# Performance work log

Measured on AMD Instinct MI355X. Metric: run time of the kernel, lower is better.

Reference implementation:

```python
import jax, jax.numpy as jnp
import numpy as np

D_MODEL, N_LAYER, VOCAB = 1024, 4, 50280
D_INNER, D_STATE, D_CONV, DT_RANK = 2048, 16, 4, 64
B, L = 1, 1024
EPS = 1e-5


def _rmsnorm(x, w):
    var = jnp.mean(jnp.square(x), axis=-1, keepdims=True)
    return x * jax.lax.rsqrt(var + EPS) * w


def _selective_scan(u, dt, A, Bm, Cm, Dv):
    # u, dt: [b,l,d]; A: [d,n]; Bm, Cm: [b,l,n]; Dv: [d]
    dA = jnp.exp(dt[..., None] * A)                      # [b,l,d,n]
    dBu = dt[..., None] * Bm[:, :, None, :] * u[..., None]  # [b,l,d,n]

    def step(s, x):
        dA_t, dBu_t, C_t = x
        s = s * dA_t + dBu_t                             # [b,d,n]
        y = jnp.einsum('bdn,bn->bd', s, C_t)
        return s, y

    s0 = jnp.zeros((u.shape[0], u.shape[2], A.shape[1]), u.dtype)
    xs = (dA.transpose(1, 0, 2, 3), dBu.transpose(1, 0, 2, 3), Cm.transpose(1, 0, 2))
    _, ys = jax.lax.scan(step, s0, xs)                   # ys: [l,b,d]
    return ys.transpose(1, 0, 2) + u * Dv


def _mixer(x, in_w, cw, cb, xp_w, dt_w, dt_b, A_log, Dv, out_w):
    Lx = x.shape[1]
    xz = jnp.einsum('bld,ed->ble', x, in_w)              # [b,l,2*d_inner]
    xp, z = jnp.split(xz, 2, axis=-1)
    # causal depthwise conv1d, kernel size D_CONV
    xpad = jnp.pad(xp, ((0, 0), (D_CONV - 1, 0), (0, 0)))
    conv = cb + sum(xpad[:, k:k + Lx, :] * cw[:, k] for k in range(D_CONV))
    u = jax.nn.silu(conv)
    xdbl = jnp.einsum('bld,ed->ble', u, xp_w)            # [b,l,dt_rank+2n]
    dt_r = xdbl[..., :DT_RANK]
    Bm = xdbl[..., DT_RANK:DT_RANK + D_STATE]
    Cm = xdbl[..., DT_RANK + D_STATE:]
    dt = jax.nn.softplus(jnp.einsum('blr,dr->bld', dt_r, dt_w) + dt_b)
    A = -jnp.exp(A_log)
    y = _selective_scan(u, dt, A, Bm, Cm, Dv)
    y = y * jax.nn.silu(z)
    return jnp.einsum('bld,ed->ble', y, out_w)


def _forward(input_ids, embedding, norm_w, in_proj_w, conv_w, conv_b, x_proj_w,
             dt_proj_w, dt_proj_b, A_log, D, out_proj_w, norm_f_w):
    hidden = embedding[input_ids]                        # [b,l,d_model]
    residual = None
    for i in range(N_LAYER):
        residual = hidden if residual is None else hidden + residual
        x = _rmsnorm(residual, norm_w[i])
        hidden = _mixer(x, in_proj_w[i], conv_w[i], conv_b[i], x_proj_w[i],
                        dt_proj_w[i], dt_proj_b[i], A_log[i], D[i], out_proj_w[i])
    residual = hidden + residual
    hf = _rmsnorm(residual, norm_f_w)
    # lm_head weight is tied to embedding
    return jnp.einsum('bld,vd->blv', hf, embedding)


def setup_inputs() -> dict:
    key = jax.random.key(0)
    ks = jax.random.split(key, 8)
    s = 0.02
    return {
        'input_ids': jax.random.randint(ks[0], (B, L), 0, VOCAB),
        'embedding': jax.random.normal(ks[1], (VOCAB, D_MODEL), jnp.float32) * s,
        'norm_w': jnp.ones((N_LAYER, D_MODEL), jnp.float32),
        'in_proj_w': jax.random.normal(ks[2], (N_LAYER, 2 * D_INNER, D_MODEL), jnp.float32) * s,
        'conv_w': jax.random.normal(ks[3], (N_LAYER, D_INNER, D_CONV), jnp.float32) * s,
        'conv_b': jnp.zeros((N_LAYER, D_INNER), jnp.float32),
        'x_proj_w': jax.random.normal(ks[4], (N_LAYER, DT_RANK + 2 * D_STATE, D_INNER), jnp.float32) * s,
        'dt_proj_w': jax.random.normal(ks[5], (N_LAYER, D_INNER, DT_RANK), jnp.float32) * s,
        'dt_proj_b': jnp.full((N_LAYER, D_INNER), -4.6, jnp.float32),  # softplus ~= 0.01
        'A_log': jnp.tile(jnp.log(jnp.arange(1.0, D_STATE + 1.0, dtype=jnp.float32))[None, None, :],
                          (N_LAYER, D_INNER, 1)),
        'D': jnp.ones((N_LAYER, D_INNER), jnp.float32),
        'out_proj_w': jax.random.normal(ks[6], (N_LAYER, D_MODEL, D_INNER), jnp.float32) * s,
        'norm_f_w': jnp.ones((D_MODEL,), jnp.float32),
    }


def reference(input_ids, embedding, norm_w, in_proj_w, conv_w, conv_b, x_proj_w,
              dt_proj_w, dt_proj_b, A_log, D, out_proj_w, norm_f_w):
    return _forward(input_ids, embedding, norm_w, in_proj_w, conv_w, conv_b,
                    x_proj_w, dt_proj_w, dt_proj_b, A_log, D, out_proj_w, norm_f_w)
```

## Files before the change

kernel.cpp:

```cpp
#include <hip/hip_runtime.h>
#include <hip/hip_bf16.h>

#define D_MODEL 1024
#define N_LAYER 4
#define D_INNER 2048
#define D_STATE 16
#define D_CONV  4
#define DT_RANK 64
#define SEQ_L   1024
#define VOCAB   50280
#define VOCAB_PAD 50304
#define NCHUNK  32
#define CLEN    32

typedef __attribute__((ext_vector_type(8))) short short8;
typedef __attribute__((ext_vector_type(4))) float f32x4;

typedef __attribute__((address_space(1))) const unsigned GUint;
typedef __attribute__((address_space(3))) unsigned LUint;

__device__ __forceinline__ float silu_f(float x) {
    return x / (1.0f + __expf(-x));
}
__device__ __forceinline__ float softplus_f(float x) {
    return fmaxf(x, 0.0f) + log1pf(__expf(-fabsf(x)));
}
__device__ __forceinline__ ushort f2bf(float f) {
    union { float f; unsigned u; } uf; uf.f = f;
    unsigned r = uf.u + 0x7FFF + ((uf.u >> 16) & 1);
    return (ushort)(r >> 16);
}

__global__ void f32_to_bf16_kernel(const float* __restrict__ in,
                                   ushort* __restrict__ out, int n4) {
    int i = blockIdx.x * 256 + threadIdx.x;
    if (i >= n4) return;
    float4 v = *(const float4*)(in + (size_t)i * 4);
    ushort4 o;
    o.x = f2bf(v.x); o.y = f2bf(v.y); o.z = f2bf(v.z); o.w = f2bf(v.w);
    *(ushort4*)(out + (size_t)i * 4) = o;
}

__global__ void xpw_convert_kernel(const float* __restrict__ src,
                                   ushort* __restrict__ dst) {
    int q = blockIdx.x * 256 + threadIdx.x;
    int layer = q / (128 * 512);
    int rq    = q % (128 * 512);
    int row   = rq / 512;
    int cq    = rq % 512;
    ushort4 o;
    if (row < 96) {
        float4 v = *(const float4*)(src + ((size_t)layer * 96 + row) * 2048 + cq * 4);
        o.x = f2bf(v.x); o.y = f2bf(v.y); o.z = f2bf(v.z); o.w = f2bf(v.w);
    } else {
        o.x = o.y = o.z = o.w = 0;
    }
    *(ushort4*)(dst + (size_t)q * 4) = o;
}

__global__ void zero_kernel(float* __restrict__ p, int n4) {
    int i = blockIdx.x * 256 + threadIdx.x;
    if (i < n4) *(float4*)(p + (size_t)i * 4) = make_float4(0.f, 0.f, 0.f, 0.f);
}

__global__ void embed_kernel(const int* __restrict__ ids,
                             const float* __restrict__ emb,
                             float* __restrict__ hidden) {
    int l = blockIdx.x;
    int t = threadIdx.x;
    int id = ids[l];
    float4 v = *(const float4*)(emb + (size_t)id * D_MODEL + t * 4);
    *(float4*)(hidden + (size_t)l * D_MODEL + t * 4) = v;
}

__global__ void add_rmsnorm_kernel(float* __restrict__ res,
                                   const float* __restrict__ h,
                                   const float* __restrict__ w,
                                   ushort* __restrict__ xout,
                                   int add) {
    int l = blockIdx.x;
    int t = threadIdx.x;
    size_t base = (size_t)l * D_MODEL + t * 4;
    float4 hv = *(const float4*)(h + base);
    float4 r;
    if (add) {
        r = *(const float4*)(res + base);
        r.x += hv.x; r.y += hv.y; r.z += hv.z; r.w += hv.w;
    } else {
        r = hv;
    }
    *(float4*)(res + base) = r;
    float ss = r.x * r.x + r.y * r.y + r.z * r.z + r.w * r.w;
    #pragma unroll
    for (int off = 32; off > 0; off >>= 1) ss += __shfl_down(ss, off, 64);
    __shared__ float sred[4];
    if ((t & 63) == 0) sred[t >> 6] = ss;
    __syncthreads();
    float tot = sred[0] + sred[1] + sred[2] + sred[3];
    float scale = rsqrtf(tot * (1.0f / (float)D_MODEL) + 1e-5f);
    float4 wv = *(const float4*)(w + t * 4);
    ushort4 o;
    o.x = f2bf(r.x * scale * wv.x);
    o.y = f2bf(r.y * scale * wv.y);
    o.z = f2bf(r.z * scale * wv.z);
    o.w = f2bf(r.w * scale * wv.w);
    *(ushort4*)(xout + base) = o;
}

template<int ATOMIC>
__global__ void gemm_bf16_gld_kernel(const ushort* __restrict__ A,
                                     const ushort* __restrict__ W,
                                     float* __restrict__ C,
                                     int N, int K, int lda, int ldc,
                                     int MB, int KS) {
    __shared__ ushort As[2][128][32];
    __shared__ ushort Ws[2][128][32];
    const int t  = threadIdx.x;
    const int T  = gridDim.x >> 3;
    const int id = blockIdx.x;
    const int j  = (id & 7) * T + (id >> 3);
    const int ks  = j % KS;
    const int rem = j / KS;
    const int m0 = (rem % MB) * 128;
    const int n0 = (rem / MB) * 128;
    const int kchunk = K / KS;
    const int kbeg = ks * kchunk;
    const int kend = kbeg + kchunk;

    const int lane = t & 63;
    const int w    = t >> 6;
    const int srow = w * 16 + (lane >> 2);
    const int scol = (lane & 3) * 8;
    const ushort* Ag0 = A + (size_t)(m0 + srow) * lda + scol;
    const ushort* Ag1 = A + (size_t)(m0 + srow + 64) * lda + scol;
    const ushort* Wg0 = W + (size_t)(n0 + srow) * K + scol;
    const ushort* Wg1 = W + (size_t)(n0 + srow + 64) * K + scol;

    const int wm = (t >> 7) & 1;
    const int wn = (t >> 6) & 1;
    const int lr = lane & 15;
    const int lk = lane >> 4;

    f32x4 acc[4][4] = {};

#define STAGE_GLD(buf, kk)                                                        \
    do {                                                                          \
        __builtin_amdgcn_global_load_lds((GUint*)(Ag0 + (kk)),                    \
            (LUint*)&As[buf][w * 16][0], 16, 0, 0);                               \
        __builtin_amdgcn_global_load_lds((GUint*)(Ag1 + (kk)),                    \
            (LUint*)&As[buf][64 + w * 16][0], 16, 0, 0);                          \
        __builtin_amdgcn_global_load_lds((GUint*)(Wg0 + (kk)),                    \
            (LUint*)&Ws[buf][w * 16][0], 16, 0, 0);                               \
        __builtin_amdgcn_global_load_lds((GUint*)(Wg1 + (kk)),                    \
            (LUint*)&Ws[buf][64 + w * 16][0], 16, 0, 0);                          \
    } while (0)

    STAGE_GLD(0, kbeg);
    int buf = 0;
    for (int k0 = kbeg;;) {
        __syncthreads();
        const bool more = (k0 + 32) < kend;
        if (more) STAGE_GLD(buf ^ 1, k0 + 32);

        short8 af[4], bfr[4];
        #pragma unroll
        for (int m = 0; m < 4; ++m)
            af[m] = *(const short8*)&As[buf][wm * 64 + m * 16 + lr][lk * 8];
        #pragma unroll
        for (int n = 0; n < 4; ++n)
            bfr[n] = *(const short8*)&Ws[buf][wn * 64 + n * 16 + lr][lk * 8];
        #pragma unroll
        for (int m = 0; m < 4; ++m)
            #pragma unroll
            for (int n = 0; n < 4; ++n)
                acc[m][n] = __builtin_amdgcn_mfma_f32_16x16x32_bf16(
                    af[m], bfr[n], acc[m][n], 0, 0, 0);

        if (!more) break;
        buf ^= 1;
        k0 += 32;
    }
#undef STAGE_GLD

    #pragma unroll
    for (int m = 0; m < 4; ++m) {
        const int row = m0 + wm * 64 + m * 16 + lk * 4;
        #pragma unroll
        for (int n = 0; n < 4; ++n) {
            const int col = n0 + wn * 64 + n * 16 + lr;
            if (col < N) {
                #pragma unroll
                for (int r = 0; r < 4; ++r) {
                    if (ATOMIC)
                        atomicAdd(&C[(size_t)(row + r) * ldc + col], acc[m][n][r]);
                    else
                        C[(size_t)(row + r) * ldc + col] = acc[m][n][r];
                }
            }
        }
    }
}

template<int EPI>
__global__ void gemm_tn_kernel(const float* __restrict__ A,
                               const float* __restrict__ W,
                               const float* __restrict__ bias,
                               float* __restrict__ C,
                               int M, int N, int K, int lda) {
    __shared__ float As[16][68];
    __shared__ float Ws[16][68];
    const int t  = threadIdx.x;
    const int m0 = blockIdx.y * 64;
    const int n0 = blockIdx.x * 64;
    const int lrow = t >> 2;
    const int lkq  = (t & 3) * 4;
    const int tx = t & 15;
    const int ty = t >> 4;

    const float* Arow = A + (size_t)(m0 + lrow) * lda;
    const int   wr    = n0 + lrow;
    const bool  wvalid = wr < N;
    const float* Wrow = W + (size_t)(wvalid ? wr : 0) * K;

    float acc[4][4] = {};
    for (int k0 = 0; k0 < K; k0 += 16) {
        float4 av = *(const float4*)(Arow + k0 + lkq);
        float4 wv = wvalid ? *(const float4*)(Wrow + k0 + lkq)
                           : make_float4(0.f, 0.f, 0.f, 0.f);
        As[lkq + 0][lrow] = av.x; As[lkq + 1][lrow] = av.y;
        As[lkq + 2][lrow] = av.z; As[lkq + 3][lrow] = av.w;
        Ws[lkq + 0][lrow] = wv.x; Ws[lkq + 1][lrow] = wv.y;
        Ws[lkq + 2][lrow] = wv.z; Ws[lkq + 3][lrow] = wv.w;
        __syncthreads();
        #pragma unroll
        for (int kk = 0; kk < 16; ++kk) {
            float4 a = *(const float4*)&As[kk][ty * 4];
            float4 b = *(const float4*)&Ws[kk][tx * 4];
            #pragma unroll
            for (int i = 0; i < 4; ++i) {
                float ai = (i == 0) ? a.x : (i == 1) ? a.y : (i == 2) ? a.z : a.w;
                acc[i][0] = fmaf(ai, b.x, acc[i][0]);
                acc[i][1] = fmaf(ai, b.y, acc[i][1]);
                acc[i][2] = fmaf(ai, b.z, acc[i][2]);
                acc[i][3] = fmaf(ai, b.w, acc[i][3]);
            }
        }
        __syncthreads();
    }

    const int colb = n0 + tx * 4;
    if (colb < N) {
        #pragma unroll
        for (int i = 0; i < 4; ++i) {
            int row = m0 + ty * 4 + i;
            float4 v = make_float4(acc[i][0], acc[i][1], acc[i][2], acc[i][3]);
            if (EPI == 1) {
                v.x = softplus_f(v.x + bias[colb + 0]);
                v.y = softplus_f(v.y + bias[colb + 1]);
                v.z = softplus_f(v.z + bias[colb + 2]);
                v.w = softplus_f(v.w + bias[colb + 3]);
            }
            *(float4*)(C + (size_t)row * N + colb) = v;
        }
    }
}

__global__ void conv_silu_kernel(const float* __restrict__ xz,
                                 const float* __restrict__ cw,
                                 const float* __restrict__ cb,
                                 float* __restrict__ u,
                                 ushort* __restrict__ u_b) {
    int idx = blockIdx.x * 256 + threadIdx.x;
    int l = idx >> 11;
    int c = idx & 2047;
    float acc = cb[c];
    float w0 = cw[c * 4 + 0], w1 = cw[c * 4 + 1], w2 = cw[c * 4 + 2], w3 = cw[c * 4 + 3];
    if (l >= 3) acc = fmaf(xz[(size_t)(l - 3) * 4096 + c], w0, acc);
    if (l >= 2) acc = fmaf(xz[(size_t)(l - 2) * 4096 + c], w1, acc);
    if (l >= 1) acc = fmaf(xz[(size_t)(l - 1) * 4096 + c], w2, acc);
    acc = fmaf(xz[(size_t)l * 4096 + c], w3, acc);
    float s = silu_f(acc);
    u[idx] = s;
    u_b[idx] = f2bf(s);
}

__global__ void scan_a_kernel(const float* __restrict__ u,
                              const float* __restrict__ dt,
                              const float* __restrict__ xdbl,
                              const float* __restrict__ A_log,
                              float* __restrict__ yloc,
                              float* __restrict__ cumdt,
                              float* __restrict__ s_end) {
    const int idx = blockIdx.x * 256 + threadIdx.x;
    const int d = idx & 2047;
    const int c = idx >> 11;

    float Aa[16];
    #pragma unroll
    for (int q = 0; q < 4; ++q) {
        float4 al = *(const float4*)(A_log + (size_t)d * 16 + q * 4);
        Aa[q * 4 + 0] = -__expf(al.x);
        Aa[q * 4 + 1] = -__expf(al.y);
        Aa[q * 4 + 2] = -__expf(al.z);
        Aa[q * 4 + 3] = -__expf(al.w);
    }

    float s[16];
    #pragma unroll
    for (int n = 0; n < 16; ++n) s[n] = 0.0f;
    float cd = 0.0f;

    const int l0 = c * CLEN;
    for (int i = 0; i < CLEN; ++i) {
        const int l = l0 + i;
        const float dtl = dt[(size_t)l * 2048 + d];
        const float ul  = u[(size_t)l * 2048 + d];
        float Bn[16], Cn[16];
        const float* xbp = xdbl + (size_t)l * 96;
        *(float4*)&Bn[0]  = *(const float4*)(xbp + 64);
        *(float4*)&Bn[4]  = *(const float4*)(xbp + 68);
        *(float4*)&Bn[8]  = *(const float4*)(xbp + 72);
        *(float4*)&Bn[12] = *(const float4*)(xbp + 76);
        *(float4*)&Cn[0]  = *(const float4*)(xbp + 80);
        *(float4*)&Cn[4]  = *(const float4*)(xbp + 84);
        *(float4*)&Cn[8]  = *(const float4*)(xbp + 88);
        *(float4*)&Cn[12] = *(const float4*)(xbp + 92);
        cd += dtl;
        const float dtu = dtl * ul;
        float y = 0.0f;
        #pragma unroll
        for (int n = 0; n < 16; ++n) {
            float dA = __expf(dtl * Aa[n]);
            s[n] = fmaf(s[n], dA, dtu * Bn[n]);
            y = fmaf(s[n], Cn[n], y);
        }
        yloc[(size_t)l * 4096 + d] = y;
        cumdt[(size_t)l * 2048 + d] = cd;
    }
    float* se = s_end + ((size_t)d * NCHUNK + c) * 16;
    #pragma unroll
    for (int q = 0; q < 4; ++q)
        *(float4*)(se + q * 4) = make_float4(s[q * 4], s[q * 4 + 1], s[q * 4 + 2], s[q * 4 + 3]);
}

__global__ void scan_b_kernel(const float* __restrict__ s_end,
                              const float* __restrict__ cumdt,
                              const float* __restrict__ A_log,
                              float* __restrict__ s_in) {
    const int idx = blockIdx.x * 256 + threadIdx.x;
    const int d = idx >> 4;
    const int n = idx & 15;
    const float Aa = -__expf(A_log[(size_t)d * 16 + n]);
    float s = 0.0f;
    #pragma unroll
    for (int c = 0; c < NCHUNK; ++c) {
        s_in[((size_t)d * NCHUNK + c) * 16 + n] = s;
        const float tot = cumdt[(size_t)(c * CLEN + CLEN - 1) * 2048 + d];
        s = s_end[((size_t)d * NCHUNK + c) * 16 + n] + __expf(Aa * tot) * s;
    }
}

__global__ void scan_c_kernel(const float* __restrict__ u,
                              const float* __restrict__ xdbl,
                              const float* __restrict__ A_log,
                              const float* __restrict__ Dv,
                              const float* __restrict__ xz,
                              const float* __restrict__ cumdt,
                              const float* __restrict__ s_in,
                              ushort* __restrict__ yb) {
    const int idx = blockIdx.x * 256 + threadIdx.x;
    const int l = idx >> 11;
    const int d = idx & 2047;
    const int c = l >> 5;

    const float cd = cumdt[idx];
    const float ul = u[idx];
    const float yv = xz[(size_t)l * 4096 + d];
    const float zv = xz[(size_t)l * 4096 + 2048 + d];
    const float* Cp = xdbl + (size_t)l * 96 + 80;
    const float* si = s_in + ((size_t)d * NCHUNK + c) * 16;

    float corr = 0.0f;
    #pragma unroll
    for (int q = 0; q < 4; ++q) {
        float4 al = *(const float4*)(A_log + (size_t)d * 16 + q * 4);
        float4 cv = *(const float4*)(Cp + q * 4);
        float4 sv = *(const float4*)(si + q * 4);
        corr = fmaf(cv.x * __expf(-__expf(al.x) * cd), sv.x, corr);
        corr = fmaf(cv.y * __expf(-__expf(al.y) * cd), sv.y, corr);
        corr = fmaf(cv.z * __expf(-__expf(al.z) * cd), sv.z, corr);
        corr = fmaf(cv.w * __expf(-__expf(al.w) * cd), sv.w, corr);
    }
    const float y = (yv + corr + Dv[d] * ul) * silu_f(zv);
    yb[idx] = f2bf(y);
}

extern "C" void kernel_launch(void* const* d_in, const int* in_sizes, int n_in,
                              void* d_out, int out_size, void* d_ws, size_t ws_size,
                              hipStream_t stream) {
    const int*   ids        = (const int*)d_in[0];
    const float* emb        = (const float*)d_in[1];
    const float* norm_w     = (const float*)d_in[2];
    const float* in_proj_w  = (const float*)d_in[3];
    const float* conv_w     = (const float*)d_in[4];
    const float* conv_b     = (const float*)d_in[5];
    const float* x_proj_w   = (const float*)d_in[6];
    const float* dt_proj_w  = (const float*)d_in[7];
    const float* dt_proj_b  = (const float*)d_in[8];
    const float* A_log      = (const float*)d_in[9];
    const float* Dv         = (const float*)d_in[10];
    const float* out_proj_w = (const float*)d_in[11];
    const float* norm_f_w   = (const float*)d_in[12];
    float* out = (float*)d_out;

    char* p = (char*)d_ws;
    ushort* emb_b  = (ushort*)p; p += (size_t)VOCAB_PAD * D_MODEL * 2;
    ushort* inw_b  = (ushort*)p; p += (size_t)N_LAYER * 4096 * 1024 * 2;
    ushort* outw_b = (ushort*)p; p += (size_t)N_LAYER * 1024 * 2048 * 2;
    ushort* xpw_b  = (ushort*)p; p += (size_t)N_LAYER * 128 * 2048 * 2;
    float* residual = (float*)p; p += (size_t)SEQ_L * D_MODEL * 4;
    float* hidden   = (float*)p; p += (size_t)SEQ_L * D_MODEL * 4;
    float* xdbl     = (float*)p; p += (size_t)SEQ_L * 96 * 4;
    ushort* xb      = (ushort*)p; p += (size_t)SEQ_L * D_MODEL * 2;
    float* xz       = (float*)p; p += (size_t)SEQ_L * 4096 * 4;
    float* u        = (float*)p; p += (size_t)SEQ_L * 2048 * 4;
    ushort* u_b     = (ushort*)p; p += (size_t)SEQ_L * 2048 * 2;
    float* dtb      = (float*)p; p += (size_t)SEQ_L * 2048 * 4;
    ushort* yb      = (ushort*)p; p += (size_t)SEQ_L * 2048 * 2;
    float* cumdt    = (float*)p; p += (size_t)SEQ_L * 2048 * 4;
    float* s_end    = (float*)p; p += (size_t)D_INNER * NCHUNK * 16 * 4;
    float* s_in     = (float*)p; p += (size_t)D_INNER * NCHUNK * 16 * 4;

    dim3 blk(256);

    f32_to_bf16_kernel<<<dim3(VOCAB * D_MODEL / 4 / 256), blk, 0, stream>>>(
        emb, emb_b, VOCAB * D_MODEL / 4);
    f32_to_bf16_kernel<<<dim3(N_LAYER * 4096 * 1024 / 4 / 256), blk, 0, stream>>>(
        in_proj_w, inw_b, N_LAYER * 4096 * 1024 / 4);
    f32_to_bf16_kernel<<<dim3(N_LAYER * 1024 * 2048 / 4 / 256), blk, 0, stream>>>(
        out_proj_w, outw_b, N_LAYER * 1024 * 2048 / 4);
    xpw_convert_kernel<<<dim3(N_LAYER * 128 * 2048 / 4 / 256), blk, 0, stream>>>(
        x_proj_w, xpw_b);

    embed_kernel<<<dim3(SEQ_L), blk, 0, stream>>>(ids, emb, hidden);

    for (int i = 0; i < N_LAYER; ++i) {
        add_rmsnorm_kernel<<<dim3(SEQ_L), blk, 0, stream>>>(
            residual, hidden, norm_w + (size_t)i * D_MODEL, xb, i == 0 ? 0 : 1);

        zero_kernel<<<dim3((SEQ_L * D_MODEL + SEQ_L * 96) / 4 / 256), blk, 0, stream>>>(
            hidden, (SEQ_L * D_MODEL + SEQ_L * 96) / 4);

        gemm_bf16_gld_kernel<0><<<dim3(256), blk, 0, stream>>>(
            xb, inw_b + (size_t)i * 4096 * 1024, xz, 4096, 1024, 1024, 4096, 8, 1);

        conv_silu_kernel<<<dim3(SEQ_L * D_INNER / 256), blk, 0, stream>>>(
            xz, conv_w + (size_t)i * D_INNER * D_CONV, conv_b + (size_t)i * D_INNER,
            u, u_b);

        gemm_bf16_gld_kernel<1><<<dim3(128), blk, 0, stream>>>(
            u_b, xpw_b + (size_t)i * 128 * 2048, xdbl, 96, 2048, 2048, 96, 8, 16);

        gemm_tn_kernel<1><<<dim3(D_INNER / 64, SEQ_L / 64), blk, 0, stream>>>(
            xdbl, dt_proj_w + (size_t)i * D_INNER * DT_RANK,
            dt_proj_b + (size_t)i * D_INNER, dtb,
            SEQ_L, D_INNER, DT_RANK, 96);

        scan_a_kernel<<<dim3(D_INNER * NCHUNK / 256), blk, 0, stream>>>(
            u, dtb, xdbl, A_log + (size_t)i * D_INNER * D_STATE, xz, cumdt, s_end);
        scan_b_kernel<<<dim3(D_INNER * 16 / 256), blk, 0, stream>>>(
            s_end, cumdt, A_log + (size_t)i * D_INNER * D_STATE, s_in);
        scan_c_kernel<<<dim3(SEQ_L * D_INNER / 256), blk, 0, stream>>>(
            u, xdbl, A_log + (size_t)i * D_INNER * D_STATE,
            Dv + (size_t)i * D_INNER, xz, cumdt, s_in, yb);

        gemm_bf16_gld_kernel<1><<<dim3(256), blk, 0, stream>>>(
            yb, outw_b + (size_t)i * 1024 * 2048, hidden, 1024, 2048, 2048, 1024, 8, 4);
    }

    add_rmsnorm_kernel<<<dim3(SEQ_L), blk, 0, stream>>>(
        residual, hidden, norm_f_w, xb, 1);

    gemm_bf16_gld_kernel<0><<<dim3(3144), blk, 0, stream>>>(
        xb, emb_b, out, VOCAB, 1024, 1024, VOCAB, 8, 1);
}
```

Before: 846.0 us.

## Replace split-K atomics with partial buffers and add LDS XOR swizzle

The split-K GEMMs now write per-split partial tiles to separate buffers instead of issuing float atomicAdds, so the zeroing kernel can go. Partials are summed in the following rmsnorm (out_proj) or in a new small reduction kernel (x_proj). The GEMM's LDS layout also gets an XOR swizzle on the k-column to reduce bank conflicts on fragment reads. The cost is extra memory traffic: four full hidden-sized partial buffers are written and read each layer, plus one extra kernel launch per layer.

```diff
diff --git a/kernel.cpp b/kernel.cpp
--- a/kernel.cpp
+++ b/kernel.cpp
@@ -58,11 +58,6 @@
     *(ushort4*)(dst + (size_t)q * 4) = o;
 }
 
-__global__ void zero_kernel(float* __restrict__ p, int n4) {
-    int i = blockIdx.x * 256 + threadIdx.x;
-    if (i < n4) *(float4*)(p + (size_t)i * 4) = make_float4(0.f, 0.f, 0.f, 0.f);
-}
-
 __global__ void embed_kernel(const int* __restrict__ ids,
                              const float* __restrict__ emb,
                              float* __restrict__ hidden) {
@@ -74,20 +69,19 @@
 }
 
 __global__ void add_rmsnorm_kernel(float* __restrict__ res,
-                                   const float* __restrict__ h,
+                                   const float* __restrict__ part,
                                    const float* __restrict__ w,
                                    ushort* __restrict__ xout,
-                                   int add) {
+                                   int add, int nparts) {
     int l = blockIdx.x;
     int t = threadIdx.x;
     size_t base = (size_t)l * D_MODEL + t * 4;
-    float4 hv = *(const float4*)(h + base);
     float4 r;
-    if (add) {
-        r = *(const float4*)(res + base);
+    if (add) r = *(const float4*)(res + base);
+    else     r = make_float4(0.f, 0.f, 0.f, 0.f);
+    for (int s = 0; s < nparts; ++s) {
+        float4 hv = *(const float4*)(part + (size_t)s * SEQ_L * D_MODEL + base);
         r.x += hv.x; r.y += hv.y; r.z += hv.z; r.w += hv.w;
-    } else {
-        r = hv;
     }
     *(float4*)(res + base) = r;
     float ss = r.x * r.x + r.y * r.y + r.z * r.z + r.w * r.w;
@@ -107,12 +101,12 @@
     *(ushort4*)(xout + base) = o;
 }
 
-template<int ATOMIC>
+template<int SPLIT>
 __global__ void gemm_bf16_gld_kernel(const ushort* __restrict__ A,
                                      const ushort* __restrict__ W,
                                      float* __restrict__ C,
                                      int N, int K, int lda, int ldc,
-                                     int MB, int KS) {
+                                     int MB, int KS, int pstride) {
     __shared__ ushort As[2][128][32];
     __shared__ ushort Ws[2][128][32];
     const int t  = threadIdx.x;
@@ -130,7 +124,7 @@
     const int lane = t & 63;
     const int w    = t >> 6;
     const int srow = w * 16 + (lane >> 2);
-    const int scol = (lane & 3) * 8;
+    const int scol = (((lane & 3) ^ ((lane >> 3) & 3)) * 8);
     const ushort* Ag0 = A + (size_t)(m0 + srow) * lda + scol;
     const ushort* Ag1 = A + (size_t)(m0 + srow + 64) * lda + scol;
     const ushort* Wg0 = W + (size_t)(n0 + srow) * K + scol;
@@ -140,6 +134,7 @@
     const int wn = (t >> 6) & 1;
     const int lr = lane & 15;
     const int lk = lane >> 4;
+    const int swz = (lr >> 1) & 3;
 
     f32x4 acc[4][4] = {};
 
@@ -165,10 +160,10 @@
         short8 af[4], bfr[4];
         #pragma unroll
         for (int m = 0; m < 4; ++m)
-            af[m] = *(const short8*)&As[buf][wm * 64 + m * 16 + lr][lk * 8];
+            af[m] = *(const short8*)&As[buf][wm * 64 + m * 16 + lr][(lk ^ swz) * 8];
         #pragma unroll
         for (int n = 0; n < 4; ++n)
-            bfr[n] = *(const short8*)&Ws[buf][wn * 64 + n * 16 + lr][lk * 8];
+            bfr[n] = *(const short8*)&Ws[buf][wn * 64 + n * 16 + lr][(lk ^ swz) * 8];
         #pragma unroll
         for (int m = 0; m < 4; ++m)
             #pragma unroll
@@ -182,6 +177,7 @@
     }
 #undef STAGE_GLD
 
+    float* Cp = SPLIT ? (C + (size_t)ks * pstride) : C;
     #pragma unroll
     for (int m = 0; m < 4; ++m) {
         const int row = m0 + wm * 64 + m * 16 + lk * 4;
@@ -190,15 +186,23 @@
             const int col = n0 + wn * 64 + n * 16 + lr;
             if (col < N) {
                 #pragma unroll
-                for (int r = 0; r < 4; ++r) {
-                    if (ATOMIC)
-                        atomicAdd(&C[(size_t)(row + r) * ldc + col], acc[m][n][r]);
-                    else
-                        C[(size_t)(row + r) * ldc + col] = acc[m][n][r];
-                }
+                for (int r = 0; r < 4; ++r)
+                    Cp[(size_t)(row + r) * ldc + col] = acc[m][n][r];
             }
         }
     }
+}
+
+__global__ void xdbl_reduce_kernel(const float* __restrict__ part,
+                                   float* __restrict__ out) {
+    int i = blockIdx.x * 256 + threadIdx.x;
+    float4 acc = make_float4(0.f, 0.f, 0.f, 0.f);
+    #pragma unroll
+    for (int s = 0; s < 16; ++s) {
+        float4 v = *(const float4*)(part + (size_t)s * SEQ_L * 96 + (size_t)i * 4);
+        acc.x += v.x; acc.y += v.y; acc.z += v.z; acc.w += v.w;
+    }
+    *(float4*)(out + (size_t)i * 4) = acc;
 }
 
 template<int EPI>
@@ -419,7 +423,8 @@
     ushort* outw_b = (ushort*)p; p += (size_t)N_LAYER * 1024 * 2048 * 2;
     ushort* xpw_b  = (ushort*)p; p += (size_t)N_LAYER * 128 * 2048 * 2;
     float* residual = (float*)p; p += (size_t)SEQ_L * D_MODEL * 4;
-    float* hidden   = (float*)p; p += (size_t)SEQ_L * D_MODEL * 4;
+    float* hpart    = (float*)p; p += (size_t)4 * SEQ_L * D_MODEL * 4;
+    float* xdpart   = (float*)p; p += (size_t)16 * SEQ_L * 96 * 4;
     float* xdbl     = (float*)p; p += (size_t)SEQ_L * 96 * 4;
     ushort* xb      = (ushort*)p; p += (size_t)SEQ_L * D_MODEL * 2;
     float* xz       = (float*)p; p += (size_t)SEQ_L * 4096 * 4;
@@ -442,24 +447,25 @@
     xpw_convert_kernel<<<dim3(N_LAYER * 128 * 2048 / 4 / 256), blk, 0, stream>>>(
         x_proj_w, xpw_b);
 
-    embed_kernel<<<dim3(SEQ_L), blk, 0, stream>>>(ids, emb, hidden);
+    embed_kernel<<<dim3(SEQ_L), blk, 0, stream>>>(ids, emb, hpart);
 
     for (int i = 0; i < N_LAYER; ++i) {
         add_rmsnorm_kernel<<<dim3(SEQ_L), blk, 0, stream>>>(
-            residual, hidden, norm_w + (size_t)i * D_MODEL, xb, i == 0 ? 0 : 1);
-
-        zero_kernel<<<dim3((SEQ_L * D_MODEL + SEQ_L * 96) / 4 / 256), blk, 0, stream>>>(
-            hidden, (SEQ_L * D_MODEL + SEQ_L * 96) / 4);
+            residual, hpart, norm_w + (size_t)i * D_MODEL, xb,
+            i == 0 ? 0 : 1, i == 0 ? 1 : 4);
 
         gemm_bf16_gld_kernel<0><<<dim3(256), blk, 0, stream>>>(
-            xb, inw_b + (size_t)i * 4096 * 1024, xz, 4096, 1024, 1024, 4096, 8, 1);
+            xb, inw_b + (size_t)i * 4096 * 1024, xz, 4096, 1024, 1024, 4096, 8, 1, 0);
 
         conv_silu_kernel<<<dim3(SEQ_L * D_INNER / 256), blk, 0, stream>>>(
             xz, conv_w + (size_t)i * D_INNER * D_CONV, conv_b + (size_t)i * D_INNER,
             u, u_b);
 
         gemm_bf16_gld_kernel<1><<<dim3(128), blk, 0, stream>>>(
-            u_b, xpw_b + (size_t)i * 128 * 2048, xdbl, 96, 2048, 2048, 96, 8, 16);
+            u_b, xpw_b + (size_t)i * 128 * 2048, xdpart, 96, 2048, 2048, 96,
+            8, 16, SEQ_L * 96);
+        xdbl_reduce_kernel<<<dim3(SEQ_L * 96 / 4 / 256), blk, 0, stream>>>(
+            xdpart, xdbl);
 
         gemm_tn_kernel<1><<<dim3(D_INNER / 64, SEQ_L / 64), blk, 0, stream>>>(
             xdbl, dt_proj_w + (size_t)i * D_INNER * DT_RANK,
@@ -475,12 +481,13 @@
             Dv + (size_t)i * D_INNER, xz, cumdt, s_in, yb);
 
         gemm_bf16_gld_kernel<1><<<dim3(256), blk, 0, stream>>>(
-            yb, outw_b + (size_t)i * 1024 * 2048, hidden, 1024, 2048, 2048, 1024, 8, 4);
+            yb, outw_b + (size_t)i * 1024 * 2048, hpart, 1024, 2048, 2048, 1024,
+            8, 4, SEQ_L * D_MODEL);
     }
 
     add_rmsnorm_kernel<<<dim3(SEQ_L), blk, 0, stream>>>(
-        residual, hidden, norm_f_w, xb, 1);
+        residual, hpart, norm_f_w, xb, 1, 4);
 
     gemm_bf16_gld_kernel<0><<<dim3(3144), blk, 0, stream>>>(
-        xb, emb_b, out, VOCAB, 1024, 1024, VOCAB, 8, 1);
-}
+        xb, emb_b, out, VOCAB, 1024, 1024, VOCAB, 8, 1, 0);
+}
```

After: 801.4 us. 5.3% less time.
